# Kernel tuning notes

Hardware: AMD Instinct MI355X
Metric: run time of the kernel (lower is better)

Reference implementation:

```python
import math
import jax, jax.numpy as jnp
import numpy as np

B, T, D, H, KVH = 2, 2048, 2048, 16, 4
DK = D // H  # 128


def setup_inputs() -> dict:
    key = jax.random.key(0)
    ks = jax.random.split(key, 7)
    q = jax.random.normal(ks[0], (B, T, D), dtype=jnp.float32)
    k = jax.random.normal(ks[1], (B, T, D), dtype=jnp.float32)
    v = jax.random.normal(ks[2], (B, T, D), dtype=jnp.float32)
    # torch Linear weights: (out_features, in_features)
    Wq = jax.random.normal(ks[3], (D, D), dtype=jnp.float32) * 0.02
    Wk = jax.random.normal(ks[4], (KVH * DK, D), dtype=jnp.float32) * 0.02
    Wv = jax.random.normal(ks[5], (KVH * DK, D), dtype=jnp.float32) * 0.02
    Wo = jax.random.normal(ks[6], (D, D), dtype=jnp.float32) * 0.02
    # qk_norm gain, init = log(max_seq_len)
    g = jnp.full((1, H, 1, 1), math.log(2048.0), dtype=jnp.float32)
    return {"q": q, "k": k, "v": v, "Wq": Wq, "Wk": Wk, "Wv": Wv, "Wo": Wo, "g": g}


def _l2norm(x, eps=1e-12):
    # matches torch F.normalize(dim=-1): x / max(||x||, eps)
    n = jnp.sqrt(jnp.sum(x * x, axis=-1, keepdims=True))
    return x / jnp.maximum(n, eps)


def reference(q, k, v, Wq, Wk, Wv, Wo, g):
    b, tq, d = q.shape
    tk = k.shape[1]
    h = g.shape[1]
    dk = d // h
    kvh = Wk.shape[0] // dk

    Q = jnp.einsum('btd,ed->bte', q, Wq).reshape(b, tq, h, dk).transpose(0, 2, 1, 3)     # (B,H,Tq,dk)
    K = jnp.einsum('btd,ed->bte', k, Wk).reshape(b, tk, kvh, dk).transpose(0, 2, 1, 3)   # (B,KVH,Tk,dk)
    V = jnp.einsum('btd,ed->bte', v, Wv).reshape(b, tk, kvh, dk).transpose(0, 2, 1, 3)

    # QK-norm + learned per-head gain
    Q = g * _l2norm(Q)
    K = _l2norm(K)

    # GQA: repeat-interleave kv heads to match query heads (torch enable_gqa)
    rep = h // kvh
    Kr = jnp.repeat(K, rep, axis=1)
    Vr = jnp.repeat(V, rep, axis=1)

    scale = 1.0 / math.sqrt(dk)
    scores = jnp.einsum('bhqd,bhkd->bhqk', Q, Kr) * scale  # (B,H,Tq,Tk)
    causal = jnp.tril(jnp.ones((tq, tk), dtype=bool))
    scores = jnp.where(causal, scores, jnp.finfo(scores.dtype).min)
    A = jax.nn.softmax(scores, axis=-1)
    Y = jnp.einsum('bhqk,bhkd->bhqd', A, Vr)               # (B,H,Tq,dk)
    Y = Y.transpose(0, 2, 1, 3).reshape(b, tq, d)
    return jnp.einsum('btd,ed->bte', Y, Wo)
```

## Files before the change

### kernel.cpp

```cpp
#include <hip/hip_runtime.h>
#include <hip/hip_bf16.h>
#include <stdint.h>

#define B_ 2
#define T_ 2048
#define D_ 2048
#define H_ 16
#define KVH_ 4
#define DK_ 128

typedef __bf16 bf16x8 __attribute__((ext_vector_type(8)));
typedef float f32x4 __attribute__((ext_vector_type(4)));
typedef unsigned short u16x8 __attribute__((ext_vector_type(8)));

typedef __attribute__((address_space(1))) void* gas1_t;
typedef __attribute__((address_space(3))) void* gas3_t;

__device__ __forceinline__ uint16_t f2bf(float f) {
  uint32_t u = __builtin_bit_cast(uint32_t, f);
  u += 0x7FFFu + ((u >> 16) & 1u);
  return (uint16_t)(u >> 16);
}

__device__ __forceinline__ void async16(const void* g, void* l) {
  __builtin_amdgcn_global_load_lds((gas1_t)(uintptr_t)g, (gas3_t)l, 16, 0, 0);
}

__global__ __launch_bounds__(256) void k_cvt_all(const float* __restrict__ q,
                                                 const float* __restrict__ k,
                                                 const float* __restrict__ v,
                                                 const float* __restrict__ wq,
                                                 const float* __restrict__ wk,
                                                 const float* __restrict__ wv,
                                                 const float* __restrict__ wo,
                                                 uint16_t* __restrict__ qb,
                                                 uint16_t* __restrict__ kb,
                                                 uint16_t* __restrict__ vb,
                                                 uint16_t* __restrict__ wqb,
                                                 uint16_t* __restrict__ wkb,
                                                 uint16_t* __restrict__ wvb,
                                                 uint16_t* __restrict__ wob) {
  int gb = blockIdx.x;
  const float* s; uint16_t* d; int base;
  if (gb < 4096)        { s = q;  d = qb;  base = 0; }
  else if (gb < 8192)   { s = k;  d = kb;  base = 4096; }
  else if (gb < 12288)  { s = v;  d = vb;  base = 8192; }
  else if (gb < 14336)  { s = wq; d = wqb; base = 12288; }
  else if (gb < 14848)  { s = wk; d = wkb; base = 14336; }
  else if (gb < 15360)  { s = wv; d = wvb; base = 14848; }
  else                  { s = wo; d = wob; base = 15360; }
  int i = (gb - base) * 256 + threadIdx.x;
  const float4* s4 = (const float4*)s;
  float4 a = s4[(size_t)i * 2], b = s4[(size_t)i * 2 + 1];
  union { uint16_t u[8]; uint4 v; } o;
  o.u[0] = f2bf(a.x); o.u[1] = f2bf(a.y); o.u[2] = f2bf(a.z); o.u[3] = f2bf(a.w);
  o.u[4] = f2bf(b.x); o.u[5] = f2bf(b.y); o.u[6] = f2bf(b.z); o.u[7] = f2bf(b.w);
  ((uint4*)d)[i] = o.v;
}


__global__ __launch_bounds__(256) void k_gemm_bt(const uint16_t* __restrict__ A,
                                                 const uint16_t* __restrict__ Bm,
                                                 float* __restrict__ C,
                                                 int M, int N, int K) {
  __shared__ uint16_t As[128 * 64];
  __shared__ uint16_t Bs[128 * 64];
  const int tid = threadIdx.x;
  const int nt = N >> 7;
  const int m0 = (blockIdx.x / nt) << 7;
  const int n0 = (blockIdx.x % nt) << 7;
  const int w = tid >> 6, lane = tid & 63;
  const int wr = (w >> 1) << 6, wc = (w & 1) << 6;
  const int lr = lane & 15;
  const int g16 = ((lane >> 4) << 4);
  const int csw = ((lane & 1) << 6) | (((lane >> 1) & 1) << 5);
  f32x4 acc[4][4] = {};
  const int soff = tid * 16;
  const int scol = ((tid & 7) ^ (((tid >> 3) & 1) << 2) ^ (((tid >> 4) & 1) << 1)) << 3;
  const int srow = tid >> 3;
  for (int kt = 0; kt < K; kt += 64) {
#pragma unroll
    for (int i = 0; i < 4; ++i) {
      int off = i * 4096 + soff;
      int row = i * 32 + srow;
      async16(A + (size_t)(m0 + row) * K + kt + scol, (char*)As + off);
      async16(Bm + (size_t)(n0 + row) * K + kt + scol, (char*)Bs + off);
    }
    __syncthreads();
#pragma unroll
    for (int kk2 = 0; kk2 < 128; kk2 += 64) {
      bf16x8 af[4], bfr[4];
      const int cb = (kk2 + g16) ^ csw;
#pragma unroll
      for (int m = 0; m < 4; ++m)
        af[m] = *(const bf16x8*)((const char*)As + (wr + m * 16 + lr) * 128 + cb);
#pragma unroll
      for (int n = 0; n < 4; ++n)
        bfr[n] = *(const bf16x8*)((const char*)Bs + (wc + n * 16 + lr) * 128 + cb);
#pragma unroll
      for (int m = 0; m < 4; ++m)
#pragma unroll
        for (int n = 0; n < 4; ++n)
          acc[m][n] = __builtin_amdgcn_mfma_f32_16x16x32_bf16(af[m], bfr[n], acc[m][n], 0, 0, 0);
    }
    __syncthreads();
  }
  const int r0 = (lane >> 4) << 2;
  const int c = lane & 15;
#pragma unroll
  for (int m = 0; m < 4; ++m)
#pragma unroll
    for (int n = 0; n < 4; ++n)
#pragma unroll
      for (int r = 0; r < 4; ++r)
        C[(size_t)(m0 + wr + m * 16 + r0 + r) * N + n0 + wc + n * 16 + c] = acc[m][n][r];
}

__global__ __launch_bounds__(256) void k_proj(const uint16_t* __restrict__ qb,
                                              const uint16_t* __restrict__ kb,
                                              const uint16_t* __restrict__ vb,
                                              const uint16_t* __restrict__ Wqb,
                                              const uint16_t* __restrict__ Wkb,
                                              const uint16_t* __restrict__ Wvb,
                                              uint16_t* __restrict__ Qn,
                                              uint16_t* __restrict__ Kn,
                                              uint16_t* __restrict__ Vt,
                                              const float* __restrict__ g) {
  __shared__ uint16_t smem[16896];
  __shared__ float ssred[2][128];
  uint16_t* As = smem;
  uint16_t* Bs = smem + 8192;
  const int bid = blockIdx.x;
  int mode, lb;
  if (bid < 128)      { mode = 2; lb = bid; }
  else if (bid < 256) { mode = 1; lb = bid - 128; }
  else                { mode = 0; lb = bid - 256; }
  const uint16_t* A;
  const uint16_t* Bw;
  int nt;
  if (mode == 0)      { A = qb; Bw = Wqb; nt = 16; }
  else if (mode == 1) { A = kb; Bw = Wkb; nt = 4; }
  else                { A = vb; Bw = Wvb; nt = 4; }
  const int K = 2048;
  const int m0 = (lb / nt) << 7;
  const int n0 = (lb % nt) << 7;
  const int tid = threadIdx.x;
  const int w = tid >> 6, lane = tid & 63;
  const int wr = (w >> 1) << 6, wc = (w & 1) << 6;
  const int lr = lane & 15;
  const int g16 = ((lane >> 4) << 4);
  const int csw = ((lane & 1) << 6) | (((lane >> 1) & 1) << 5);
  f32x4 acc[4][4] = {};
  const int soff = tid * 16;
  const int scol = ((tid & 7) ^ (((tid >> 3) & 1) << 2) ^ (((tid >> 4) & 1) << 1)) << 3;
  const int srow = tid >> 3;
  for (int kt = 0; kt < K; kt += 64) {
#pragma unroll
    for (int i = 0; i < 4; ++i) {
      int off = i * 4096 + soff;
      int row = i * 32 + srow;
      async16(A + (size_t)(m0 + row) * K + kt + scol, (char*)As + off);
      async16(Bw + (size_t)(n0 + row) * K + kt + scol, (char*)Bs + off);
    }
    __syncthreads();
#pragma unroll
    for (int kk2 = 0; kk2 < 128; kk2 += 64) {
      bf16x8 af[4], bfr[4];
      const int cb = (kk2 + g16) ^ csw;
#pragma unroll
      for (int m = 0; m < 4; ++m)
        af[m] = *(const bf16x8*)((const char*)As + (wr + m * 16 + lr) * 128 + cb);
#pragma unroll
      for (int n = 0; n < 4; ++n)
        bfr[n] = *(const bf16x8*)((const char*)Bs + (wc + n * 16 + lr) * 128 + cb);
#pragma unroll
      for (int m = 0; m < 4; ++m)
#pragma unroll
        for (int n = 0; n < 4; ++n)
          acc[m][n] = __builtin_amdgcn_mfma_f32_16x16x32_bf16(af[m], bfr[n], acc[m][n], 0, 0, 0);
    }
    __syncthreads();
  }
  const int g4 = lane >> 4;
  const int r04 = g4 << 2;
  const int b = m0 >> 11;
  const int t0 = m0 & (T_ - 1);
  const int h = n0 >> 7;

  if (mode <= 1) {
    float ss[4][4];
#pragma unroll
    for (int m = 0; m < 4; ++m)
#pragma unroll
      for (int r = 0; r < 4; ++r) {
        float s = 0.f;
#pragma unroll
        for (int n = 0; n < 4; ++n) s += acc[m][n][r] * acc[m][n][r];
        ss[m][r] = s;
      }
#pragma unroll
    for (int mask = 1; mask < 16; mask <<= 1)
#pragma unroll
      for (int m = 0; m < 4; ++m)
#pragma unroll
        for (int r = 0; r < 4; ++r) ss[m][r] += __shfl_xor(ss[m][r], mask);
#pragma unroll
    for (int m = 0; m < 4; ++m)
#pragma unroll
      for (int r = 0; r < 4; ++r)
        if (lr == (m << 2 | r)) ssred[w & 1][wr + m * 16 + g4 * 4 + r] = ss[m][r];
    __syncthreads();
    uint16_t* outp = (mode == 0) ? Qn : Kn;
    const int NHv = (mode == 0) ? H_ : KVH_;
    const float gmul = (mode == 0) ? g[h] * 0.08838834764831845f : 1.0f;
#pragma unroll
    for (int m = 0; m < 4; ++m)
#pragma unroll
      for (int r = 0; r < 4; ++r) {
        int row = wr + m * 16 + g4 * 4 + r;
        float tot = ssred[0][row] + ssred[1][row];
        float scl = gmul / fmaxf(sqrtf(tot), 1e-12f);
        size_t base = ((size_t)(b * NHv + h) * T_ + (t0 + row)) * 128;
#pragma unroll
        for (int n = 0; n < 4; ++n)
          outp[base + wc + n * 16 + lr] = f2bf(acc[m][n][r] * scl);
      }
  } else {
    uint16_t* tr = smem;
#pragma unroll
    for (int m = 0; m < 4; ++m)
#pragma unroll
      for (int n = 0; n < 4; ++n)
#pragma unroll
        for (int r = 0; r < 4; ++r)
          tr[(wc + n * 16 + lr) * 132 + (wr + m * 16 + r04 + r)] = f2bf(acc[m][n][r]);
    __syncthreads();
    const int qd = tid & 3;
#pragma unroll
    for (int dd = 0; dd < 2; ++dd) {
      int d = (tid >> 2) + dd * 64;
      uint16_t* dst = Vt + ((size_t)(b * KVH_ + h) * 128 + d) * T_ + t0 + qd * 32;
      const uint16_t* srcl = &tr[d * 132 + qd * 32];
#pragma unroll
      for (int j = 0; j < 8; ++j)
        *(ushort4*)(dst + j * 4) = *(const ushort4*)(srcl + j * 4);
    }
  }
}

__global__ __launch_bounds__(256) void k_attn(const uint16_t* __restrict__ Qn,
                                              const uint16_t* __restrict__ Kn,
                                              const uint16_t* __restrict__ Vt,
                                              uint16_t* __restrict__ Y) {
  __shared__ uint16_t Ks[64 * 128];
  __shared__ uint16_t Vs[128 * 64];
  __shared__ uint16_t Ps[4 * 16 * 32];
  const int npair = T_ / 128;
  const int pair_id = blockIdx.x % npair;
  const int bh = blockIdx.x / npair;
  const int h = bh % H_;
  const int b = bh / H_;
  const int kvh = h >> 2;
  const int qtA = pair_id;
  const int qtB = (T_ / 64) - 1 - pair_id;
  const uint16_t* Qh = Qn + ((size_t)(b * H_ + h) * T_) * 128;
  const uint16_t* Kh = Kn + ((size_t)(b * KVH_ + kvh) * T_) * 128;
  const uint16_t* Vh = Vt + ((size_t)(b * KVH_ + kvh) * 128) * T_;
  const int tid = threadIdx.x;
  const int w = tid >> 6, lane = tid & 63;
  const int lr = lane & 15;
  const int lk2 = (lane >> 4) << 4;
  const int r0 = (lane >> 4) << 2;
  const int qwA = qtA * 64 + w * 16;
  const int qwB = qtB * 64 + w * 16;
  char* Psw = (char*)Ps + w * 1024;

  bf16x8 qfA[4], qfB[4];
#pragma unroll
  for (int dblk = 0; dblk < 4; ++dblk) {
    qfA[dblk] = *(const bf16x8*)&Qh[(size_t)(qwA + lr) * 128 + dblk * 32 + (lk2 >> 1)];
    qfB[dblk] = *(const bf16x8*)&Qh[(size_t)(qwB + lr) * 128 + dblk * 32 + (lk2 >> 1)];
  }
  union { uint16_t u[8]; bf16x8 v; } ou;
#pragma unroll
  for (int j = 0; j < 8; ++j) ou.u[j] = 0x3F80;
  const bf16x8 ones = ou.v;
  f32x4 oA[8] = {}, oB[8] = {};
  f32x4 sumA = {}, sumB = {};

  auto tilecompute = [&](const bf16x8* qf, f32x4* o, f32x4* sum, int qw, int kv0) {
#pragma unroll
    for (int prr = 0; prr < 2; ++prr) {
#pragma unroll
      for (int kbi = 0; kbi < 2; ++kbi) {
        int kb = prr * 2 + kbi;
        f32x4 s = {};
#pragma unroll
        for (int dblk = 0; dblk < 4; ++dblk) {
          bf16x8 kf = *(const bf16x8*)((const char*)Ks +
              ((kb * 16 + lr) << 8) + ((dblk * 64 + lk2) ^ ((lr & 7) << 4)));
          s = __builtin_amdgcn_mfma_f32_16x16x32_bf16(qf[dblk], kf, s, 0, 0, 0);
        }
        int kval = kv0 + kb * 16 + lr;
#pragma unroll
        for (int r = 0; r < 4; ++r) {
          float pv = (kval <= qw + r0 + r) ? __expf(s[r]) : 0.0f;
          *(uint16_t*)(Psw + (r0 + r) * 64 + (((kbi * 16 + lr) * 2) ^ (r << 4))) = f2bf(pv);
        }
      }
      asm volatile("s_waitcnt lgkmcnt(0)" ::: "memory");
      bf16x8 pa = *(const bf16x8*)(Psw + lr * 64 + (lk2 ^ ((lr & 3) << 4)));
#pragma unroll
      for (int dblk = 0; dblk < 8; ++dblk) {
        bf16x8 vf = *(const bf16x8*)((const char*)Vs +
            ((dblk * 16 + lr) << 7) + ((prr * 64 + lk2) ^ ((lr & 7) << 4)));
        o[dblk] = __builtin_amdgcn_mfma_f32_16x16x32_bf16(pa, vf, o[dblk], 0, 0, 0);
      }
      *sum = __builtin_amdgcn_mfma_f32_16x16x32_bf16(pa, ones, *sum, 0, 0, 0);
    }
  };

  for (int tile = 0; tile <= qtB; ++tile) {
    const int kv0 = tile * 64;
#pragma unroll
    for (int i = 0; i < 4; ++i) {
      int off = i * 4096 + tid * 16;
      int krow = off >> 8;
      int kchunk = (off >> 4) & 15;
      int kcol = (kchunk ^ (krow & 7)) << 3;
      async16(Kh + (size_t)(kv0 + krow) * 128 + kcol, (char*)Ks + off);
      int vrow = off >> 7;
      int vchunk = (off >> 4) & 7;
      int vcol = (vchunk ^ (vrow & 7)) << 3;
      async16(Vh + (size_t)vrow * T_ + kv0 + vcol, (char*)Vs + off);
    }
    __syncthreads();
    tilecompute(qfB, oB, &sumB, qwB, kv0);
    if (tile <= qtA) tilecompute(qfA, oA, &sumA, qwA, kv0);
    __syncthreads();
  }

  auto writeout = [&](const f32x4* o, const f32x4& sum, int qw) {
#pragma unroll
    for (int r = 0; r < 4; ++r) {
      float inv = 1.0f / sum[r];
      size_t base = ((size_t)b * T_ + (qw + r0 + r)) * D_ + h * 128 + lr;
#pragma unroll
      for (int dblk = 0; dblk < 8; ++dblk)
        Y[base + dblk * 16] = f2bf(o[dblk][r] * inv);
    }
  };
  writeout(oA, sumA, qwA);
  writeout(oB, sumB, qwB);
}

extern "C" void kernel_launch(void* const* d_in, const int* in_sizes, int n_in,
                              void* d_out, int out_size, void* d_ws, size_t ws_size,
                              hipStream_t stream) {
  (void)in_sizes; (void)n_in; (void)out_size; (void)ws_size;
  const float* q  = (const float*)d_in[0];
  const float* k  = (const float*)d_in[1];
  const float* v  = (const float*)d_in[2];
  const float* Wq = (const float*)d_in[3];
  const float* Wk = (const float*)d_in[4];
  const float* Wv = (const float*)d_in[5];
  const float* Wo = (const float*)d_in[6];
  const float* g  = (const float*)d_in[7];
  float* out = (float*)d_out;
  char* ws = (char*)d_ws;
  const size_t MB = 1ull << 20;
  uint16_t* qb  = (uint16_t*)(ws);
  uint16_t* kb  = (uint16_t*)(ws + 16 * MB);
  uint16_t* vb  = (uint16_t*)(ws + 32 * MB);
  uint16_t* Wqb = (uint16_t*)(ws + 48 * MB);
  uint16_t* Wkb = (uint16_t*)(ws + 56 * MB);
  uint16_t* Wvb = (uint16_t*)(ws + 58 * MB);
  uint16_t* Kn  = (uint16_t*)(ws + 60 * MB);
  uint16_t* Vtb = (uint16_t*)(ws + 64 * MB);
  uint16_t* Wob = (uint16_t*)(ws + 68 * MB);
  uint16_t* Qn  = (uint16_t*)d_out;
  uint16_t* Y   = qb;

  k_cvt_all<<<17408, 256, 0, stream>>>(q, k, v, Wq, Wk, Wv, Wo,
                                       qb, kb, vb, Wqb, Wkb, Wvb, Wob);
  k_proj<<<768, 256, 0, stream>>>(qb, kb, vb, Wqb, Wkb, Wvb, Qn, Kn, Vtb, g);
  k_attn<<<B_ * H_ * (T_ / 128), 256, 0, stream>>>(Qn, Kn, Vtb, Y);
  k_gemm_bt<<<(B_ * T_ / 128) * (D_ / 128), 256, 0, stream>>>(Y, Wob, out, B_ * T_, D_, D_);
}
```

Measured before the change: 230.8 us.

## Fuse activation fp32->bf16 conversion into projection and double-buffer LDS in all GEMMs

Activation conversion moves out of the standalone convert kernel and into the projection GEMM, which now loads fp32 activations into registers, converts them and writes bf16 to LDS. This removes a full write and re-read of the bf16 copies of q, k and v. The output GEMM, the projection weight tiles and the attention K/V tiles are now double-buffered, so the next tile's loads overlap the current tile's MFMAs. In exchange, LDS use grows, which can lower occupancy, and the projection kernel issues more non-async global loads through registers.

After: 288.7 us. 25.1% more time.

```diff
diff --git a/kernel.cpp b/kernel.cpp
--- a/kernel.cpp
+++ b/kernel.cpp
@@ -26,29 +26,20 @@
   __builtin_amdgcn_global_load_lds((gas1_t)(uintptr_t)g, (gas3_t)l, 16, 0, 0);
 }
 
-__global__ __launch_bounds__(256) void k_cvt_all(const float* __restrict__ q,
-                                                 const float* __restrict__ k,
-                                                 const float* __restrict__ v,
-                                                 const float* __restrict__ wq,
-                                                 const float* __restrict__ wk,
-                                                 const float* __restrict__ wv,
-                                                 const float* __restrict__ wo,
-                                                 uint16_t* __restrict__ qb,
-                                                 uint16_t* __restrict__ kb,
-                                                 uint16_t* __restrict__ vb,
-                                                 uint16_t* __restrict__ wqb,
-                                                 uint16_t* __restrict__ wkb,
-                                                 uint16_t* __restrict__ wvb,
-                                                 uint16_t* __restrict__ wob) {
+__global__ __launch_bounds__(256) void k_cvt_w(const float* __restrict__ wq,
+                                               const float* __restrict__ wk,
+                                               const float* __restrict__ wv,
+                                               const float* __restrict__ wo,
+                                               uint16_t* __restrict__ wqb,
+                                               uint16_t* __restrict__ wkb,
+                                               uint16_t* __restrict__ wvb,
+                                               uint16_t* __restrict__ wob) {
   int gb = blockIdx.x;
   const float* s; uint16_t* d; int base;
-  if (gb < 4096)        { s = q;  d = qb;  base = 0; }
-  else if (gb < 8192)   { s = k;  d = kb;  base = 4096; }
-  else if (gb < 12288)  { s = v;  d = vb;  base = 8192; }
-  else if (gb < 14336)  { s = wq; d = wqb; base = 12288; }
-  else if (gb < 14848)  { s = wk; d = wkb; base = 14336; }
-  else if (gb < 15360)  { s = wv; d = wvb; base = 14848; }
-  else                  { s = wo; d = wob; base = 15360; }
+  if (gb < 2048)       { s = wq; d = wqb; base = 0; }
+  else if (gb < 2560)  { s = wk; d = wkb; base = 2048; }
+  else if (gb < 3072)  { s = wv; d = wvb; base = 2560; }
+  else                 { s = wo; d = wob; base = 3072; }
   int i = (gb - base) * 256 + threadIdx.x;
   const float4* s4 = (const float4*)s;
   float4 a = s4[(size_t)i * 2], b = s4[(size_t)i * 2 + 1];
@@ -63,8 +54,8 @@
                                                  const uint16_t* __restrict__ Bm,
                                                  float* __restrict__ C,
                                                  int M, int N, int K) {
-  __shared__ uint16_t As[128 * 64];
-  __shared__ uint16_t Bs[128 * 64];
+  __shared__ uint16_t As[2 * 128 * 64];
+  __shared__ uint16_t Bs[2 * 128 * 64];
   const int tid = threadIdx.x;
   const int nt = N >> 7;
   const int m0 = (blockIdx.x / nt) << 7;
@@ -78,32 +69,45 @@
   const int soff = tid * 16;
   const int scol = ((tid & 7) ^ (((tid >> 3) & 1) << 2) ^ (((tid >> 4) & 1) << 1)) << 3;
   const int srow = tid >> 3;
-  for (int kt = 0; kt < K; kt += 64) {
+  const int nk = K >> 6;
+
+  auto stage = [&](int t, int buf) {
+    char* Ab = (char*)As + (buf << 14);
+    char* Bb = (char*)Bs + (buf << 14);
 #pragma unroll
     for (int i = 0; i < 4; ++i) {
-      int off = i * 4096 + soff;
       int row = i * 32 + srow;
-      async16(A + (size_t)(m0 + row) * K + kt + scol, (char*)As + off);
-      async16(Bm + (size_t)(n0 + row) * K + kt + scol, (char*)Bs + off);
-    }
-    __syncthreads();
+      async16(A + (size_t)(m0 + row) * K + t * 64 + scol, Ab + i * 4096 + soff);
+      async16(Bm + (size_t)(n0 + row) * K + t * 64 + scol, Bb + i * 4096 + soff);
+    }
+  };
+
+  stage(0, 0);
+  asm volatile("s_waitcnt vmcnt(0)" ::: "memory");
+  __builtin_amdgcn_s_barrier();
+  for (int t = 0; t < nk; ++t) {
+    const int cur = t & 1;
+    if (t + 1 < nk) stage(t + 1, cur ^ 1);
+    const char* Ab = (const char*)As + (cur << 14);
+    const char* Bb = (const char*)Bs + (cur << 14);
 #pragma unroll
     for (int kk2 = 0; kk2 < 128; kk2 += 64) {
       bf16x8 af[4], bfr[4];
       const int cb = (kk2 + g16) ^ csw;
 #pragma unroll
       for (int m = 0; m < 4; ++m)
-        af[m] = *(const bf16x8*)((const char*)As + (wr + m * 16 + lr) * 128 + cb);
+        af[m] = *(const bf16x8*)(Ab + (wr + m * 16 + lr) * 128 + cb);
 #pragma unroll
       for (int n = 0; n < 4; ++n)
-        bfr[n] = *(const bf16x8*)((const char*)Bs + (wc + n * 16 + lr) * 128 + cb);
+        bfr[n] = *(const bf16x8*)(Bb + (wc + n * 16 + lr) * 128 + cb);
 #pragma unroll
       for (int m = 0; m < 4; ++m)
 #pragma unroll
         for (int n = 0; n < 4; ++n)
           acc[m][n] = __builtin_amdgcn_mfma_f32_16x16x32_bf16(af[m], bfr[n], acc[m][n], 0, 0, 0);
     }
-    __syncthreads();
+    asm volatile("s_waitcnt vmcnt(0)" ::: "memory");
+    __builtin_amdgcn_s_barrier();
   }
   const int r0 = (lane >> 4) << 2;
   const int c = lane & 15;
@@ -116,9 +120,9 @@
         C[(size_t)(m0 + wr + m * 16 + r0 + r) * N + n0 + wc + n * 16 + c] = acc[m][n][r];
 }
 
-__global__ __launch_bounds__(256) void k_proj(const uint16_t* __restrict__ qb,
-                                              const uint16_t* __restrict__ kb,
-                                              const uint16_t* __restrict__ vb,
+__global__ __launch_bounds__(256) void k_proj(const float* __restrict__ qf32,
+                                              const float* __restrict__ kf32,
+                                              const float* __restrict__ vf32,
                                               const uint16_t* __restrict__ Wqb,
                                               const uint16_t* __restrict__ Wkb,
                                               const uint16_t* __restrict__ Wvb,
@@ -126,22 +130,19 @@
                                               uint16_t* __restrict__ Kn,
                                               uint16_t* __restrict__ Vt,
                                               const float* __restrict__ g) {
-  __shared__ uint16_t smem[16896];
+  __shared__ char smem[49152];
   __shared__ float ssred[2][128];
-  uint16_t* As = smem;
-  uint16_t* Bs = smem + 8192;
   const int bid = blockIdx.x;
   int mode, lb;
   if (bid < 128)      { mode = 2; lb = bid; }
   else if (bid < 256) { mode = 1; lb = bid - 128; }
   else                { mode = 0; lb = bid - 256; }
-  const uint16_t* A;
+  const float* A32;
   const uint16_t* Bw;
   int nt;
-  if (mode == 0)      { A = qb; Bw = Wqb; nt = 16; }
-  else if (mode == 1) { A = kb; Bw = Wkb; nt = 4; }
-  else                { A = vb; Bw = Wvb; nt = 4; }
-  const int K = 2048;
+  if (mode == 0)      { A32 = qf32; Bw = Wqb; nt = 16; }
+  else if (mode == 1) { A32 = kf32; Bw = Wkb; nt = 4; }
+  else                { A32 = vf32; Bw = Wvb; nt = 4; }
   const int m0 = (lb / nt) << 7;
   const int n0 = (lb % nt) << 7;
   const int tid = threadIdx.x;
@@ -154,33 +155,68 @@
   const int soff = tid * 16;
   const int scol = ((tid & 7) ^ (((tid >> 3) & 1) << 2) ^ (((tid >> 4) & 1) << 1)) << 3;
   const int srow = tid >> 3;
-  for (int kt = 0; kt < K; kt += 64) {
+
+  float4 fa[8];
+  auto loadA = [&](int t) {
+    const float* base = A32 + (size_t)(m0 + srow) * 2048 + t * 64 + scol;
 #pragma unroll
     for (int i = 0; i < 4; ++i) {
-      int off = i * 4096 + soff;
-      int row = i * 32 + srow;
-      async16(A + (size_t)(m0 + row) * K + kt + scol, (char*)As + off);
-      async16(Bw + (size_t)(n0 + row) * K + kt + scol, (char*)Bs + off);
-    }
-    __syncthreads();
+      fa[i * 2]     = *(const float4*)(base + (size_t)i * 32 * 2048);
+      fa[i * 2 + 1] = *(const float4*)(base + (size_t)i * 32 * 2048 + 4);
+    }
+  };
+  auto writeA = [&]() {
+#pragma unroll
+    for (int i = 0; i < 4; ++i) {
+      union { uint16_t u[8]; u16x8 v8; } o;
+      float4 a = fa[i * 2], b = fa[i * 2 + 1];
+      o.u[0] = f2bf(a.x); o.u[1] = f2bf(a.y); o.u[2] = f2bf(a.z); o.u[3] = f2bf(a.w);
+      o.u[4] = f2bf(b.x); o.u[5] = f2bf(b.y); o.u[6] = f2bf(b.z); o.u[7] = f2bf(b.w);
+      *(u16x8*)(smem + i * 4096 + soff) = o.v8;
+    }
+  };
+  auto stageB = [&](int t, int buf) {
+    char* base = smem + 16384 + (buf << 14);
+#pragma unroll
+    for (int i = 0; i < 4; ++i)
+      async16(Bw + (size_t)(n0 + i * 32 + srow) * 2048 + t * 64 + scol,
+              base + i * 4096 + soff);
+  };
+
+  loadA(0);
+  writeA();
+  stageB(0, 0);
+  asm volatile("s_waitcnt vmcnt(0) lgkmcnt(0)" ::: "memory");
+  __builtin_amdgcn_s_barrier();
+
+  for (int t = 0; t < 32; ++t) {
+    const int cur = t & 1;
+    if (t < 31) { loadA(t + 1); stageB(t + 1, cur ^ 1); }
+    const char* Bb = (const char*)smem + 16384 + (cur << 14);
 #pragma unroll
     for (int kk2 = 0; kk2 < 128; kk2 += 64) {
       bf16x8 af[4], bfr[4];
       const int cb = (kk2 + g16) ^ csw;
 #pragma unroll
       for (int m = 0; m < 4; ++m)
-        af[m] = *(const bf16x8*)((const char*)As + (wr + m * 16 + lr) * 128 + cb);
+        af[m] = *(const bf16x8*)(smem + (wr + m * 16 + lr) * 128 + cb);
 #pragma unroll
       for (int n = 0; n < 4; ++n)
-        bfr[n] = *(const bf16x8*)((const char*)Bs + (wc + n * 16 + lr) * 128 + cb);
+        bfr[n] = *(const bf16x8*)(Bb + (wc + n * 16 + lr) * 128 + cb);
 #pragma unroll
       for (int m = 0; m < 4; ++m)
 #pragma unroll
         for (int n = 0; n < 4; ++n)
           acc[m][n] = __builtin_amdgcn_mfma_f32_16x16x32_bf16(af[m], bfr[n], acc[m][n], 0, 0, 0);
     }
-    __syncthreads();
+    __builtin_amdgcn_s_barrier();
+    if (t < 31) {
+      writeA();
+      asm volatile("s_waitcnt vmcnt(0) lgkmcnt(0)" ::: "memory");
+    }
+    __builtin_amdgcn_s_barrier();
   }
+
   const int g4 = lane >> 4;
   const int r04 = g4 << 2;
   const int b = m0 >> 11;
@@ -226,7 +262,7 @@
           outp[base + wc + n * 16 + lr] = f2bf(acc[m][n][r] * scl);
       }
   } else {
-    uint16_t* tr = smem;
+    uint16_t* tr = (uint16_t*)smem;
 #pragma unroll
     for (int m = 0; m < 4; ++m)
 #pragma unroll
@@ -252,8 +288,8 @@
                                               const uint16_t* __restrict__ Kn,
                                               const uint16_t* __restrict__ Vt,
                                               uint16_t* __restrict__ Y) {
-  __shared__ uint16_t Ks[64 * 128];
-  __shared__ uint16_t Vs[128 * 64];
+  __shared__ uint16_t Ks[2 * 64 * 128];
+  __shared__ uint16_t Vs[2 * 128 * 64];
   __shared__ uint16_t Ps[4 * 16 * 32];
   const int npair = T_ / 128;
   const int pair_id = blockIdx.x % npair;
@@ -288,7 +324,27 @@
   f32x4 oA[8] = {}, oB[8] = {};
   f32x4 sumA = {}, sumB = {};
 
-  auto tilecompute = [&](const bf16x8* qf, f32x4* o, f32x4* sum, int qw, int kv0) {
+  auto stageKV = [&](int tile, int buf) {
+    const int kv0 = tile * 64;
+    char* Kb = (char*)Ks + (buf << 14);
+    char* Vb = (char*)Vs + (buf << 14);
+#pragma unroll
+    for (int i = 0; i < 4; ++i) {
+      int off = i * 4096 + tid * 16;
+      int krow = off >> 8;
+      int kchunk = (off >> 4) & 15;
+      int kcol = (kchunk ^ (krow & 7)) << 3;
+      async16(Kh + (size_t)(kv0 + krow) * 128 + kcol, Kb + off);
+      int vrow = off >> 7;
+      int vchunk = (off >> 4) & 7;
+      int vcol = (vchunk ^ (vrow & 7)) << 3;
+      async16(Vh + (size_t)vrow * T_ + kv0 + vcol, Vb + off);
+    }
+  };
+
+  auto tilecompute = [&](const bf16x8* qf, f32x4* o, f32x4* sum, int qw, int kv0, int cur) {
+    const char* Kb = (const char*)Ks + (cur << 14);
+    const char* Vb = (const char*)Vs + (cur << 14);
 #pragma unroll
     for (int prr = 0; prr < 2; ++prr) {
 #pragma unroll
@@ -297,7 +353,7 @@
         f32x4 s = {};
 #pragma unroll
         for (int dblk = 0; dblk < 4; ++dblk) {
-          bf16x8 kf = *(const bf16x8*)((const char*)Ks +
+          bf16x8 kf = *(const bf16x8*)(Kb +
               ((kb * 16 + lr) << 8) + ((dblk * 64 + lk2) ^ ((lr & 7) << 4)));
           s = __builtin_amdgcn_mfma_f32_16x16x32_bf16(qf[dblk], kf, s, 0, 0, 0);
         }
@@ -312,7 +368,7 @@
       bf16x8 pa = *(const bf16x8*)(Psw + lr * 64 + (lk2 ^ ((lr & 3) << 4)));
 #pragma unroll
       for (int dblk = 0; dblk < 8; ++dblk) {
-        bf16x8 vf = *(const bf16x8*)((const char*)Vs +
+        bf16x8 vf = *(const bf16x8*)(Vb +
             ((dblk * 16 + lr) << 7) + ((prr * 64 + lk2) ^ ((lr & 7) << 4)));
         o[dblk] = __builtin_amdgcn_mfma_f32_16x16x32_bf16(pa, vf, o[dblk], 0, 0, 0);
       }
@@ -320,24 +376,17 @@
     }
   };
 
+  stageKV(0, 0);
+  asm volatile("s_waitcnt vmcnt(0)" ::: "memory");
+  __builtin_amdgcn_s_barrier();
   for (int tile = 0; tile <= qtB; ++tile) {
+    const int cur = tile & 1;
+    if (tile < qtB) stageKV(tile + 1, cur ^ 1);
     const int kv0 = tile * 64;
-#pragma unroll
-    for (int i = 0; i < 4; ++i) {
-      int off = i * 4096 + tid * 16;
-      int krow = off >> 8;
-      int kchunk = (off >> 4) & 15;
-      int kcol = (kchunk ^ (krow & 7)) << 3;
-      async16(Kh + (size_t)(kv0 + krow) * 128 + kcol, (char*)Ks + off);
-      int vrow = off >> 7;
-      int vchunk = (off >> 4) & 7;
-      int vcol = (vchunk ^ (vrow & 7)) << 3;
-      async16(Vh + (size_t)vrow * T_ + kv0 + vcol, (char*)Vs + off);
-    }
-    __syncthreads();
-    tilecompute(qfB, oB, &sumB, qwB, kv0);
-    if (tile <= qtA) tilecompute(qfA, oA, &sumA, qwA, kv0);
-    __syncthreads();
+    tilecompute(qfB, oB, &sumB, qwB, kv0, cur);
+    if (tile <= qtA) tilecompute(qfA, oA, &sumA, qwA, kv0, cur);
+    asm volatile("s_waitcnt vmcnt(0)" ::: "memory");
+    __builtin_amdgcn_s_barrier();
   }
 
   auto writeout = [&](const f32x4* o, const f32x4& sum, int qw) {
@@ -369,21 +418,17 @@
   float* out = (float*)d_out;
   char* ws = (char*)d_ws;
   const size_t MB = 1ull << 20;
-  uint16_t* qb  = (uint16_t*)(ws);
-  uint16_t* kb  = (uint16_t*)(ws + 16 * MB);
-  uint16_t* vb  = (uint16_t*)(ws + 32 * MB);
-  uint16_t* Wqb = (uint16_t*)(ws + 48 * MB);
-  uint16_t* Wkb = (uint16_t*)(ws + 56 * MB);
-  uint16_t* Wvb = (uint16_t*)(ws + 58 * MB);
-  uint16_t* Kn  = (uint16_t*)(ws + 60 * MB);
-  uint16_t* Vtb = (uint16_t*)(ws + 64 * MB);
-  uint16_t* Wob = (uint16_t*)(ws + 68 * MB);
+  uint16_t* Y   = (uint16_t*)(ws);
+  uint16_t* Wqb = (uint16_t*)(ws + 16 * MB);
+  uint16_t* Wkb = (uint16_t*)(ws + 24 * MB);
+  uint16_t* Wvb = (uint16_t*)(ws + 26 * MB);
+  uint16_t* Wob = (uint16_t*)(ws + 28 * MB);
+  uint16_t* Kn  = (uint16_t*)(ws + 36 * MB);
+  uint16_t* Vtb = (uint16_t*)(ws + 40 * MB);
   uint16_t* Qn  = (uint16_t*)d_out;
-  uint16_t* Y   = qb;
-
-  k_cvt_all<<<17408, 256, 0, stream>>>(q, k, v, Wq, Wk, Wv, Wo,
-                                       qb, kb, vb, Wqb, Wkb, Wvb, Wob);
-  k_proj<<<768, 256, 0, stream>>>(qb, kb, vb, Wqb, Wkb, Wvb, Qn, Kn, Vtb, g);
+
+  k_cvt_w<<<5120, 256, 0, stream>>>(Wq, Wk, Wv, Wo, Wqb, Wkb, Wvb, Wob);
+  k_proj<<<768, 256, 0, stream>>>(q, k, v, Wqb, Wkb, Wvb, Qn, Kn, Vtb, g);
   k_attn<<<B_ * H_ * (T_ / 128), 256, 0, stream>>>(Qn, Kn, Vtb, Y);
   k_gemm_bt<<<(B_ * T_ / 128) * (D_ / 128), 256, 0, stream>>>(Y, Wob, out, B_ * T_, D_, D_);
 }
```

## Double-buffer LDS tiles in GEMM, projection and attention kernels

Applied to the files above, without the earlier changes.

Adds two-stage LDS double buffering to the output GEMM, the fused QKV projection and the attention kernel. The async global-to-LDS loads for the next K-tile or KV-tile are issued before the current tile is computed, and each iteration ends with a vmcnt wait plus a barrier. This replaces the load-then-sync-then-compute pattern and is meant to hide global memory latency behind MFMA work. It doubles shared memory per block (64KB in projection, 64KB for K/V in attention), which may reduce occupancy.

Measured after the change: 222.4 us. -3.6%, faster.

```diff
diff --git a/kernel.cpp b/kernel.cpp
--- a/kernel.cpp
+++ b/kernel.cpp
@@ -63,8 +63,8 @@
                                                  const uint16_t* __restrict__ Bm,
                                                  float* __restrict__ C,
                                                  int M, int N, int K) {
-  __shared__ uint16_t As[128 * 64];
-  __shared__ uint16_t Bs[128 * 64];
+  __shared__ uint16_t As[2 * 128 * 64];
+  __shared__ uint16_t Bs[2 * 128 * 64];
   const int tid = threadIdx.x;
   const int nt = N >> 7;
   const int m0 = (blockIdx.x / nt) << 7;
@@ -78,32 +78,45 @@
   const int soff = tid * 16;
   const int scol = ((tid & 7) ^ (((tid >> 3) & 1) << 2) ^ (((tid >> 4) & 1) << 1)) << 3;
   const int srow = tid >> 3;
-  for (int kt = 0; kt < K; kt += 64) {
+  const int nk = K >> 6;
+
+  auto stage = [&](int t, int buf) {
+    char* Ab = (char*)As + (buf << 14);
+    char* Bb = (char*)Bs + (buf << 14);
 #pragma unroll
     for (int i = 0; i < 4; ++i) {
-      int off = i * 4096 + soff;
       int row = i * 32 + srow;
-      async16(A + (size_t)(m0 + row) * K + kt + scol, (char*)As + off);
-      async16(Bm + (size_t)(n0 + row) * K + kt + scol, (char*)Bs + off);
-    }
-    __syncthreads();
+      async16(A + (size_t)(m0 + row) * K + t * 64 + scol, Ab + i * 4096 + soff);
+      async16(Bm + (size_t)(n0 + row) * K + t * 64 + scol, Bb + i * 4096 + soff);
+    }
+  };
+
+  stage(0, 0);
+  asm volatile("s_waitcnt vmcnt(0)" ::: "memory");
+  __builtin_amdgcn_s_barrier();
+  for (int t = 0; t < nk; ++t) {
+    const int cur = t & 1;
+    if (t + 1 < nk) stage(t + 1, cur ^ 1);
+    const char* Ab = (const char*)As + (cur << 14);
+    const char* Bb = (const char*)Bs + (cur << 14);
 #pragma unroll
     for (int kk2 = 0; kk2 < 128; kk2 += 64) {
       bf16x8 af[4], bfr[4];
       const int cb = (kk2 + g16) ^ csw;
 #pragma unroll
       for (int m = 0; m < 4; ++m)
-        af[m] = *(const bf16x8*)((const char*)As + (wr + m * 16 + lr) * 128 + cb);
+        af[m] = *(const bf16x8*)(Ab + (wr + m * 16 + lr) * 128 + cb);
 #pragma unroll
       for (int n = 0; n < 4; ++n)
-        bfr[n] = *(const bf16x8*)((const char*)Bs + (wc + n * 16 + lr) * 128 + cb);
+        bfr[n] = *(const bf16x8*)(Bb + (wc + n * 16 + lr) * 128 + cb);
 #pragma unroll
       for (int m = 0; m < 4; ++m)
 #pragma unroll
         for (int n = 0; n < 4; ++n)
           acc[m][n] = __builtin_amdgcn_mfma_f32_16x16x32_bf16(af[m], bfr[n], acc[m][n], 0, 0, 0);
     }
-    __syncthreads();
+    asm volatile("s_waitcnt vmcnt(0)" ::: "memory");
+    __builtin_amdgcn_s_barrier();
   }
   const int r0 = (lane >> 4) << 2;
   const int c = lane & 15;
@@ -126,10 +139,8 @@
                                               uint16_t* __restrict__ Kn,
                                               uint16_t* __restrict__ Vt,
                                               const float* __restrict__ g) {
-  __shared__ uint16_t smem[16896];
+  __shared__ char smem[65536];
   __shared__ float ssred[2][128];
-  uint16_t* As = smem;
-  uint16_t* Bs = smem + 8192;
   const int bid = blockIdx.x;
   int mode, lb;
   if (bid < 128)      { mode = 2; lb = bid; }
@@ -141,7 +152,6 @@
   if (mode == 0)      { A = qb; Bw = Wqb; nt = 16; }
   else if (mode == 1) { A = kb; Bw = Wkb; nt = 4; }
   else                { A = vb; Bw = Wvb; nt = 4; }
-  const int K = 2048;
   const int m0 = (lb / nt) << 7;
   const int n0 = (lb % nt) << 7;
   const int tid = threadIdx.x;
@@ -154,33 +164,46 @@
   const int soff = tid * 16;
   const int scol = ((tid & 7) ^ (((tid >> 3) & 1) << 2) ^ (((tid >> 4) & 1) << 1)) << 3;
   const int srow = tid >> 3;
-  for (int kt = 0; kt < K; kt += 64) {
+
+  auto stage = [&](int t, int buf) {
+    char* Ab = smem + (buf << 14);
+    char* Bb = smem + 32768 + (buf << 14);
 #pragma unroll
     for (int i = 0; i < 4; ++i) {
-      int off = i * 4096 + soff;
       int row = i * 32 + srow;
-      async16(A + (size_t)(m0 + row) * K + kt + scol, (char*)As + off);
-      async16(Bw + (size_t)(n0 + row) * K + kt + scol, (char*)Bs + off);
-    }
-    __syncthreads();
+      async16(A + (size_t)(m0 + row) * 2048 + t * 64 + scol, Ab + i * 4096 + soff);
+      async16(Bw + (size_t)(n0 + row) * 2048 + t * 64 + scol, Bb + i * 4096 + soff);
+    }
+  };
+
+  stage(0, 0);
+  asm volatile("s_waitcnt vmcnt(0)" ::: "memory");
+  __builtin_amdgcn_s_barrier();
+  for (int t = 0; t < 32; ++t) {
+    const int cur = t & 1;
+    if (t < 31) stage(t + 1, cur ^ 1);
+    const char* Ab = (const char*)smem + (cur << 14);
+    const char* Bb = (const char*)smem + 32768 + (cur << 14);
 #pragma unroll
     for (int kk2 = 0; kk2 < 128; kk2 += 64) {
       bf16x8 af[4], bfr[4];
       const int cb = (kk2 + g16) ^ csw;
 #pragma unroll
       for (int m = 0; m < 4; ++m)
-        af[m] = *(const bf16x8*)((const char*)As + (wr + m * 16 + lr) * 128 + cb);
+        af[m] = *(const bf16x8*)(Ab + (wr + m * 16 + lr) * 128 + cb);
 #pragma unroll
       for (int n = 0; n < 4; ++n)
-        bfr[n] = *(const bf16x8*)((const char*)Bs + (wc + n * 16 + lr) * 128 + cb);
+        bfr[n] = *(const bf16x8*)(Bb + (wc + n * 16 + lr) * 128 + cb);
 #pragma unroll
       for (int m = 0; m < 4; ++m)
 #pragma unroll
         for (int n = 0; n < 4; ++n)
           acc[m][n] = __builtin_amdgcn_mfma_f32_16x16x32_bf16(af[m], bfr[n], acc[m][n], 0, 0, 0);
     }
-    __syncthreads();
+    asm volatile("s_waitcnt vmcnt(0)" ::: "memory");
+    __builtin_amdgcn_s_barrier();
   }
+
   const int g4 = lane >> 4;
   const int r04 = g4 << 2;
   const int b = m0 >> 11;
@@ -226,7 +249,7 @@
           outp[base + wc + n * 16 + lr] = f2bf(acc[m][n][r] * scl);
       }
   } else {
-    uint16_t* tr = smem;
+    uint16_t* tr = (uint16_t*)smem;
 #pragma unroll
     for (int m = 0; m < 4; ++m)
 #pragma unroll
@@ -252,8 +275,8 @@
                                               const uint16_t* __restrict__ Kn,
                                               const uint16_t* __restrict__ Vt,
                                               uint16_t* __restrict__ Y) {
-  __shared__ uint16_t Ks[64 * 128];
-  __shared__ uint16_t Vs[128 * 64];
+  __shared__ uint16_t Ks[2 * 64 * 128];
+  __shared__ uint16_t Vs[2 * 128 * 64];
   __shared__ uint16_t Ps[4 * 16 * 32];
   const int npair = T_ / 128;
   const int pair_id = blockIdx.x % npair;
@@ -288,7 +311,27 @@
   f32x4 oA[8] = {}, oB[8] = {};
   f32x4 sumA = {}, sumB = {};
 
-  auto tilecompute = [&](const bf16x8* qf, f32x4* o, f32x4* sum, int qw, int kv0) {
+  auto stageKV = [&](int tile, int buf) {
+    const int kv0 = tile * 64;
+    char* Kb = (char*)Ks + (buf << 14);
+    char* Vb = (char*)Vs + (buf << 14);
+#pragma unroll
+    for (int i = 0; i < 4; ++i) {
+      int off = i * 4096 + tid * 16;
+      int krow = off >> 8;
+      int kchunk = (off >> 4) & 15;
+      int kcol = (kchunk ^ (krow & 7)) << 3;
+      async16(Kh + (size_t)(kv0 + krow) * 128 + kcol, Kb + off);
+      int vrow = off >> 7;
+      int vchunk = (off >> 4) & 7;
+      int vcol = (vchunk ^ (vrow & 7)) << 3;
+      async16(Vh + (size_t)vrow * T_ + kv0 + vcol, Vb + off);
+    }
+  };
+
+  auto tilecompute = [&](const bf16x8* qf, f32x4* o, f32x4* sum, int qw, int kv0, int cur) {
+    const char* Kb = (const char*)Ks + (cur << 14);
+    const char* Vb = (const char*)Vs + (cur << 14);
 #pragma unroll
     for (int prr = 0; prr < 2; ++prr) {
 #pragma unroll
@@ -297,7 +340,7 @@
         f32x4 s = {};
 #pragma unroll
         for (int dblk = 0; dblk < 4; ++dblk) {
-          bf16x8 kf = *(const bf16x8*)((const char*)Ks +
+          bf16x8 kf = *(const bf16x8*)(Kb +
               ((kb * 16 + lr) << 8) + ((dblk * 64 + lk2) ^ ((lr & 7) << 4)));
           s = __builtin_amdgcn_mfma_f32_16x16x32_bf16(qf[dblk], kf, s, 0, 0, 0);
         }
@@ -312,7 +355,7 @@
       bf16x8 pa = *(const bf16x8*)(Psw + lr * 64 + (lk2 ^ ((lr & 3) << 4)));
 #pragma unroll
       for (int dblk = 0; dblk < 8; ++dblk) {
-        bf16x8 vf = *(const bf16x8*)((const char*)Vs +
+        bf16x8 vf = *(const bf16x8*)(Vb +
             ((dblk * 16 + lr) << 7) + ((prr * 64 + lk2) ^ ((lr & 7) << 4)));
         o[dblk] = __builtin_amdgcn_mfma_f32_16x16x32_bf16(pa, vf, o[dblk], 0, 0, 0);
       }
@@ -320,24 +363,17 @@
     }
   };
 
+  stageKV(0, 0);
+  asm volatile("s_waitcnt vmcnt(0)" ::: "memory");
+  __builtin_amdgcn_s_barrier();
   for (int tile = 0; tile <= qtB; ++tile) {
+    const int cur = tile & 1;
+    if (tile < qtB) stageKV(tile + 1, cur ^ 1);
     const int kv0 = tile * 64;
-#pragma unroll
-    for (int i = 0; i < 4; ++i) {
-      int off = i * 4096 + tid * 16;
-      int krow = off >> 8;
-      int kchunk = (off >> 4) & 15;
-      int kcol = (kchunk ^ (krow & 7)) << 3;
-      async16(Kh + (size_t)(kv0 + krow) * 128 + kcol, (char*)Ks + off);
-      int vrow = off >> 7;
-      int vchunk = (off >> 4) & 7;
-      int vcol = (vchunk ^ (vrow & 7)) << 3;
-      async16(Vh + (size_t)vrow * T_ + kv0 + vcol, (char*)Vs + off);
-    }
-    __syncthreads();
-    tilecompute(qfB, oB, &sumB, qwB, kv0);
-    if (tile <= qtA) tilecompute(qfA, oA, &sumA, qwA, kv0);
-    __syncthreads();
+    tilecompute(qfB, oB, &sumB, qwB, kv0, cur);
+    if (tile <= qtA) tilecompute(qfA, oA, &sumA, qwA, kv0, cur);
+    asm volatile("s_waitcnt vmcnt(0)" ::: "memory");
+    __builtin_amdgcn_s_barrier();
   }
 
   auto writeout = [&](const f32x4* o, const f32x4& sum, int qw) {
```
